# Kernel tuning notes

Measured on AMD Instinct MI355X. Metric: run time of the kernel, lower is better.

The kernel has to match this reference:

```python
import jax, jax.numpy as jnp
import numpy as np

B, NE, NR, D1, D2, L = 64, 40000, 500, 200, 200, 64
BN_EPS = 1e-5


def _batchnorm(x, gamma, beta):
    # training-mode BatchNorm1d: biased batch statistics over axis 0
    mu = jnp.mean(x, axis=0)
    var = jnp.var(x, axis=0)
    return gamma * (x - mu) * jax.lax.rsqrt(var + BN_EPS) + beta


def setup_inputs() -> dict:
    key = jax.random.key(0)
    ks = jax.random.split(key, 10)
    return {
        "e1_idx": jax.random.randint(ks[0], (B,), 0, NE),
        "r_idx": jax.random.randint(ks[1], (B,), 0, NR),
        "E": jax.random.normal(ks[2], (NE, D1), dtype=jnp.float32),
        "R": jax.random.normal(ks[3], (NR, D2), dtype=jnp.float32),
        # W ~ Uniform(-1, 1) as in the torch module
        "W": jax.random.uniform(ks[4], (D2, D1, D1), dtype=jnp.float32, minval=-1.0, maxval=1.0),
        # literals normalized into [0, 1]
        "lits": jax.random.uniform(ks[5], (NE, L), dtype=jnp.float32),
        "c": jax.random.normal(ks[6], (L,), dtype=jnp.float32) * 0.1,
        # variance buffer must be positive
        "var_l": jax.random.uniform(ks[7], (L,), dtype=jnp.float32, minval=0.5, maxval=1.5),
        "nf": jax.random.normal(ks[8], (NR, L), dtype=jnp.float32) * 0.1,
        "bn0_gamma": jnp.ones((D1,), jnp.float32),
        "bn0_beta": jnp.zeros((D1,), jnp.float32),
        "bn1_gamma": jnp.ones((D1,), jnp.float32),
        "bn1_beta": jnp.zeros((D1,), jnp.float32),
    }


def reference(e1_idx, r_idx, E, R, W, lits, c, var_l, nf,
              bn0_gamma, bn0_beta, bn1_gamma, bn1_beta):
    # --- TuckER core ---
    e1 = E[e1_idx]                                   # (B, d1)
    x = _batchnorm(e1, bn0_gamma, bn0_beta)          # (B, d1)
    r = R[r_idx]                                     # (B, d2)
    W_mat = jnp.einsum('bk,kij->bij', r, W)          # (B, d1, d1)
    x = jnp.einsum('bi,bij->bj', x, W_mat)           # (B, d1)
    x = _batchnorm(x, bn1_gamma, bn1_beta)
    score_l = x @ E.T                                # (B, N)

    # --- KBLN numeric-literal branch ---
    n_h = lits[e1_idx]                               # (B, L)
    # broadcast instead of .repeat: (B, 1, L) - (1, N, L) -> (B, N, L)
    n = n_h[:, None, :] - lits[None, :, :]
    phi = jnp.exp(-jnp.square(n - c) / var_l)        # (B, N, L)
    w_nf = nf[r_idx]                                 # (B, L)
    score_n = jnp.einsum('bnl,bl->bn', phi, w_nf)    # (B, N)

    return jax.nn.sigmoid(score_l + score_n)
```

## Files before the change

### kernel.cpp

```cpp
#include <hip/hip_runtime.h>
#include <math.h>

#define BB    64
#define NEC   40000
#define NRC   500
#define D1C   200
#define D2C   200
#define LLC   64
#define BN_EPS 1e-5f
#define LOG2E 1.4426950408889634f

#define WS_XT    0
#define WS_RT    12800
#define WS_TAP   25600
#define WS_WP    29696
#define WS_SL    33792
#define WS_X2BH  33856
#define WS_X2BL  42048
#define WS_Y     50240

typedef short s8v __attribute__((ext_vector_type(8)));
typedef float f4v __attribute__((ext_vector_type(4)));

__device__ __forceinline__ unsigned short bf16_rne(float x) {
  unsigned b = __float_as_uint(x);
  unsigned r = b + 0x7FFFu + ((b >> 16) & 1u);
  return (unsigned short)(r >> 16);
}
__device__ __forceinline__ void split2(float x, unsigned short& h,
                                       unsigned short& l) {
  h = bf16_rne(x);
  float hf = __uint_as_float(((unsigned)h) << 16);
  l = bf16_rne(x - hf);
}

__global__ __launch_bounds__(256) void prep_kernel(
    const int* __restrict__ e1_idx, const int* __restrict__ r_idx,
    const float* __restrict__ E, const float* __restrict__ R,
    const float* __restrict__ lits, const float* __restrict__ c,
    const float* __restrict__ var_l, const float* __restrict__ nf,
    const float* __restrict__ bn0g, const float* __restrict__ bn0b,
    float* __restrict__ ws) {
  float* xT  = ws + WS_XT;
  float* rT  = ws + WS_RT;
  float* taP = ws + WS_TAP;
  float* wP  = ws + WS_WP;
  float* sl  = ws + WS_SL;
  int tid = threadIdx.x;

  if (blockIdx.x == 0) {
    if (tid < D1C) {
      int j = tid;
      float ev[64];
      float sum = 0.f, sq = 0.f;
#pragma unroll
      for (int b = 0; b < BB; b++) {
        float e = E[e1_idx[b] * D1C + j];
        ev[b] = e;
        sum += e; sq += e * e;
      }
      float mean = sum * (1.f / 64.f);
      float var  = sq  * (1.f / 64.f) - mean * mean;
      float inv  = __builtin_amdgcn_rsqf(var + BN_EPS);
      float g    = bn0g[j] * inv;
      float be   = bn0b[j] - mean * g;
#pragma unroll
      for (int b = 0; b < BB; b++) {
        xT[j * 64 + b] = g * ev[b] + be;
      }
    }
  } else if (blockIdx.x == 1) {
    for (int idx = tid; idx < D2C * 64; idx += 256) {
      int k = idx >> 6, b = idx & 63;
      rT[idx] = R[r_idx[b] * D2C + k];
    }
  } else if (blockIdx.x == 2) {
    for (int idx = tid; idx < LLC * 64; idx += 256) {
      int l = idx >> 6, b = idx & 63;
      float s = sqrtf(LOG2E / var_l[l]);
      float a = (lits[e1_idx[b] * LLC + l] - c[l]) * s;
      int bp = (b & 15) * 4 + (b >> 4);
      taP[l * 64 + bp] = a + a;
      wP[l * 64 + bp]  = nf[r_idx[b] * LLC + l] * __builtin_amdgcn_exp2f(-a * a);
    }
    if (tid < LLC) sl[tid] = sqrtf(LOG2E / var_l[tid]);
  } else {
    unsigned* z = (unsigned*)(ws + WS_X2BH);
    for (int i = tid; i < 16384; i += 256) z[i] = 0u;
  }
}

__global__ __launch_bounds__(512) void stage1_kernel(
    const float* __restrict__ W, const float* __restrict__ ws_in,
    float* __restrict__ y) {
  const float* xT = ws_in + WS_XT;
  const float* rT = ws_in + WS_RT;

  int k = blockIdx.x;
  int tid = threadIdx.x;
  int lane = tid & 63;
  int w = __builtin_amdgcn_readfirstlane(tid >> 6);
  int jc = w & 3, bh = w >> 2;
  int j4 = lane & 15, bq = lane >> 4;
  int j0 = jc * 64 + j4 * 4;
  int b0 = bh * 32 + bq * 8;
  bool jok = j0 < 200;
  int joff = jok ? j0 : 0;
  const float* Wk = W + k * 40000 + joff;
  const float* xp = xT + b0;

  float acc[4][8];
#pragma unroll
  for (int jj = 0; jj < 4; jj++)
#pragma unroll
    for (int bb = 0; bb < 8; bb++) acc[jj][bb] = 0.f;

#pragma unroll 4
  for (int i = 0; i < D1C; i++) {
    float4 wv  = *(const float4*)(Wk + i * 200);
    float4 xa  = *(const float4*)(xp + i * 64);
    float4 xb2 = *(const float4*)(xp + i * 64 + 4);
    float wc[4] = {wv.x, wv.y, wv.z, wv.w};
    float xv[8] = {xa.x, xa.y, xa.z, xa.w, xb2.x, xb2.y, xb2.z, xb2.w};
#pragma unroll
    for (int jj = 0; jj < 4; jj++)
#pragma unroll
      for (int bb = 0; bb < 8; bb++)
        acc[jj][bb] += wc[jj] * xv[bb];
  }

  if (jok) {
    float4 r0 = *(const float4*)(rT + k * 64 + b0);
    float4 r1 = *(const float4*)(rT + k * 64 + b0 + 4);
    float rv[8] = {r0.x, r0.y, r0.z, r0.w, r1.x, r1.y, r1.z, r1.w};
#pragma unroll
    for (int jj = 0; jj < 4; jj++) {
      float* yo = y + (k * D1C + j0 + jj) * 64 + b0;
      float4 o0 = make_float4(acc[jj][0] * rv[0], acc[jj][1] * rv[1],
                              acc[jj][2] * rv[2], acc[jj][3] * rv[3]);
      float4 o1 = make_float4(acc[jj][4] * rv[4], acc[jj][5] * rv[5],
                              acc[jj][6] * rv[6], acc[jj][7] * rv[7]);
      *(float4*)(yo) = o0;
      *(float4*)(yo + 4) = o1;
    }
  }
}

__global__ __launch_bounds__(256) void reduce_bn1_kernel(
    const float* __restrict__ y, const float* __restrict__ bn1g,
    const float* __restrict__ bn1b, float* __restrict__ ws) {
  int j = blockIdx.x;
  int tid = threadIdx.x, b = tid & 63, kq = tid >> 6;

  float s = 0.f;
  const float* yp = y + (kq * 50 * D1C + j) * 64 + b;
#pragma unroll 10
  for (int k = 0; k < 50; k++) s += yp[k * D1C * 64];

  __shared__ float part[256];
  part[tid] = s;
  __syncthreads();
  if (tid < 64) {
    float v = part[tid] + part[64 + tid] + part[128 + tid] + part[192 + tid];
    float sum = v, sq = v * v;
#pragma unroll
    for (int o = 32; o > 0; o >>= 1) {
      sum += __shfl_xor(sum, o, 64);
      sq  += __shfl_xor(sq,  o, 64);
    }
    float mean = sum * (1.f / 64.f);
    float var  = sq  * (1.f / 64.f) - mean * mean;
    float inv  = __builtin_amdgcn_rsqf(var + BN_EPS);
    float g    = bn1g[j] * inv;
    float be   = bn1b[j] - mean * g;
    float xv   = g * v + be;
    unsigned short h, l;
    split2(xv, h, l);
    unsigned short* xh = (unsigned short*)(ws + WS_X2BH);
    unsigned short* xl = (unsigned short*)(ws + WS_X2BL);
    xh[tid * 256 + j] = h;
    xl[tid * 256 + j] = l;
  }
}

__global__ __launch_bounds__(256, 4) void final_kernel(
    const float* __restrict__ E, const float* __restrict__ lits,
    const float* __restrict__ ws, float* __restrict__ out) {
  const float* taP = ws + WS_TAP;
  const float* wP  = ws + WS_WP;
  const float* sl  = ws + WS_SL;
  const unsigned short* x2bh = (const unsigned short*)(ws + WS_X2BH);
  const unsigned short* x2bl = (const unsigned short*)(ws + WS_X2BL);

  __shared__ float SM[9216];
  unsigned short* Ah = (unsigned short*)SM;
  unsigned short* Al = Ah + 4608;
  unsigned short* Bh = Ah + 9216;
  unsigned short* Bl = Ah + 13824;

  int n0 = blockIdx.x * 64;
  int tid = threadIdx.x;
  int lane = tid & 63;
  int w = __builtin_amdgcn_readfirstlane(tid >> 6);
  int ln = lane & 15;
  int quad = lane >> 4;

  f4v acc[4];
#pragma unroll
  for (int t = 0; t < 4; t++) acc[t] = (f4v){0.f, 0.f, 0.f, 0.f};

  for (int q = 0; q < 4; q++) {
    int k0 = q * 64;
    __syncthreads();
#pragma unroll
    for (int it = 0; it < 4; it++) {
      int idx = tid + it * 256;
      int row = idx >> 4, c4 = idx & 15, cc = c4 * 4;
      float4 v = make_float4(0.f, 0.f, 0.f, 0.f);
      if (k0 + cc < 200) v = *(const float4*)(E + (n0 + row) * D1C + k0 + cc);
      unsigned short h0, l0, h1, l1, h2, l2, h3, l3;
      split2(v.x, h0, l0); split2(v.y, h1, l1);
      split2(v.z, h2, l2); split2(v.w, h3, l3);
      *(ushort4*)(Ah + row * 72 + cc) = make_ushort4(h0, h1, h2, h3);
      *(ushort4*)(Al + row * 72 + cc) = make_ushort4(l0, l1, l2, l3);
    }
#pragma unroll
    for (int it = 0; it < 4; it++) {
      int idx = tid + it * 256;
      int row = idx >> 4, c4 = idx & 15;
      *(ushort4*)(Bh + row * 72 + c4 * 4) =
          *(const ushort4*)(x2bh + row * 256 + k0 + c4 * 4);
      *(ushort4*)(Bl + row * 72 + c4 * 4) =
          *(const ushort4*)(x2bl + row * 256 + k0 + c4 * 4);
    }
    __syncthreads();

    const unsigned short* Ab  = Ah + (16 * w + ln) * 72 + quad * 8;
    const unsigned short* Alb = Al + (16 * w + ln) * 72 + quad * 8;
#pragma unroll
    for (int ks = 0; ks < 64; ks += 32) {
      s8v ah = *(const s8v*)(Ab + ks);
      s8v al = *(const s8v*)(Alb + ks);
#pragma unroll
      for (int t = 0; t < 4; t++) {
        s8v bh = *(const s8v*)(Bh + (16 * t + ln) * 72 + quad * 8 + ks);
        s8v bl = *(const s8v*)(Bl + (16 * t + ln) * 72 + quad * 8 + ks);
        acc[t] = __builtin_amdgcn_mfma_f32_16x16x32_bf16(ah, bh, acc[t], 0, 0, 0);
        acc[t] = __builtin_amdgcn_mfma_f32_16x16x32_bf16(al, bh, acc[t], 0, 0, 0);
        acc[t] = __builtin_amdgcn_mfma_f32_16x16x32_bf16(ah, bl, acc[t], 0, 0, 0);
      }
    }
  }

  float* Llds = SM;
  float* TAl  = SM + 4352;
  float* Wl   = SM + 6400;
  int nlb = 16 * w + 4 * quad;

  __syncthreads();
#pragma unroll
  for (int it = 0; it < 4; it++) {
    int idx = tid + it * 256;
    int row = idx >> 4, c4 = idx & 15;
    float4 v = *(const float4*)(lits + (n0 + row) * LLC + c4 * 4);
    int l = c4 * 4;
    Llds[(l + 0) * 68 + row] = v.x * sl[l + 0];
    Llds[(l + 1) * 68 + row] = v.y * sl[l + 1];
    Llds[(l + 2) * 68 + row] = v.z * sl[l + 2];
    Llds[(l + 3) * 68 + row] = v.w * sl[l + 3];
  }

  for (int h = 0; h < 2; h++) {
    __syncthreads();
#pragma unroll
    for (int it = 0; it < 2; it++) {
      int idx = tid + it * 256;
      ((float4*)TAl)[idx] = ((const float4*)(taP + h * 2048))[idx];
      ((float4*)Wl)[idx]  = ((const float4*)(wP  + h * 2048))[idx];
    }
    __syncthreads();
    for (int ll = 0; ll < 32; ll++) {
      float4 Lv = *(const float4*)(Llds + (h * 32 + ll) * 68 + nlb);
      float4 ta = *(const float4*)(TAl + ll * 64 + 4 * ln);
      float4 wv = *(const float4*)(Wl  + ll * 64 + 4 * ln);
      float Lc[4]  = {Lv.x, Lv.y, Lv.z, Lv.w};
      float tac[4] = {ta.x, ta.y, ta.z, ta.w};
      float wvc[4] = {wv.x, wv.y, wv.z, wv.w};
      float n2[4];
#pragma unroll
      for (int r = 0; r < 4; r++) n2[r] = -Lc[r] * Lc[r];
#pragma unroll
      for (int t = 0; t < 4; t++) {
#pragma unroll
        for (int r = 0; r < 4; r++) {
          acc[t][r] += wvc[t] *
              __builtin_amdgcn_exp2f(__builtin_fmaf(tac[t], Lc[r], n2[r]));
        }
      }
    }
  }

#pragma unroll
  for (int t = 0; t < 4; t++) {
    float4 o;
    o.x = __builtin_amdgcn_rcpf(1.f + __builtin_amdgcn_exp2f(-LOG2E * acc[t][0]));
    o.y = __builtin_amdgcn_rcpf(1.f + __builtin_amdgcn_exp2f(-LOG2E * acc[t][1]));
    o.z = __builtin_amdgcn_rcpf(1.f + __builtin_amdgcn_exp2f(-LOG2E * acc[t][2]));
    o.w = __builtin_amdgcn_rcpf(1.f + __builtin_amdgcn_exp2f(-LOG2E * acc[t][3]));
    *(float4*)(out + (size_t)(16 * t + ln) * NEC + n0 + nlb) = o;
  }
}

extern "C" void kernel_launch(void* const* d_in, const int* in_sizes, int n_in,
                              void* d_out, int out_size, void* d_ws, size_t ws_size,
                              hipStream_t stream) {
  (void)in_sizes; (void)n_in; (void)out_size; (void)ws_size;
  const int*   e1    = (const int*)d_in[0];
  const int*   ri    = (const int*)d_in[1];
  const float* E     = (const float*)d_in[2];
  const float* R     = (const float*)d_in[3];
  const float* W     = (const float*)d_in[4];
  const float* lits  = (const float*)d_in[5];
  const float* c     = (const float*)d_in[6];
  const float* var_l = (const float*)d_in[7];
  const float* nf    = (const float*)d_in[8];
  const float* bn0g  = (const float*)d_in[9];
  const float* bn0b  = (const float*)d_in[10];
  const float* bn1g  = (const float*)d_in[11];
  const float* bn1b  = (const float*)d_in[12];
  float* out = (float*)d_out;
  float* ws  = (float*)d_ws;
  float* y   = ws + WS_Y;

  prep_kernel<<<4, 256, 0, stream>>>(e1, ri, E, R, lits, c, var_l, nf,
                                     bn0g, bn0b, ws);
  stage1_kernel<<<200, 512, 0, stream>>>(W, ws, y);
  reduce_bn1_kernel<<<200, 256, 0, stream>>>(y, bn1g, bn1b, ws);
  final_kernel<<<625, 256, 0, stream>>>(E, lits, ws, out);
}
```

Measured before the change: 213.2 us.

## Split stage1 reduction over i into four chunks and prefetch loads

Stage1 now launches a 200x4 grid in which each block reduces over 50 of the 200 i values and writes partial results into a y buffer four times larger. The reduce kernel widens to 512 threads and sums the 800 partials per j. A software-pipelined register prefetch of the next W and x loads is added, and launch_bounds requests more resident waves. The aim is to fill more of the GPU's CUs, since 200 blocks underuse MI355X, at the cost of four times more intermediate y traffic and register pressure from the prefetch.

```diff
diff --git a/kernel.cpp b/kernel.cpp
--- a/kernel.cpp
+++ b/kernel.cpp
@@ -90,13 +90,14 @@
   }
 }
 
-__global__ __launch_bounds__(512) void stage1_kernel(
+__global__ __launch_bounds__(512, 6) void stage1_kernel(
     const float* __restrict__ W, const float* __restrict__ ws_in,
     float* __restrict__ y) {
   const float* xT = ws_in + WS_XT;
   const float* rT = ws_in + WS_RT;
 
   int k = blockIdx.x;
+  int ih = blockIdx.y;
   int tid = threadIdx.x;
   int lane = tid & 63;
   int w = __builtin_amdgcn_readfirstlane(tid >> 6);
@@ -106,8 +107,8 @@
   int b0 = bh * 32 + bq * 8;
   bool jok = j0 < 200;
   int joff = jok ? j0 : 0;
-  const float* Wk = W + k * 40000 + joff;
-  const float* xp = xT + b0;
+  const float* Wk = W + k * 40000 + ih * 50 * 200 + joff;
+  const float* xp = xT + ih * 50 * 64 + b0;
 
   float acc[4][8];
 #pragma unroll
@@ -115,11 +116,17 @@
 #pragma unroll
     for (int bb = 0; bb < 8; bb++) acc[jj][bb] = 0.f;
 
-#pragma unroll 4
-  for (int i = 0; i < D1C; i++) {
-    float4 wv  = *(const float4*)(Wk + i * 200);
-    float4 xa  = *(const float4*)(xp + i * 64);
-    float4 xb2 = *(const float4*)(xp + i * 64 + 4);
+  float4 wv  = *(const float4*)(Wk);
+  float4 xa  = *(const float4*)(xp);
+  float4 xb2 = *(const float4*)(xp + 4);
+#pragma unroll 5
+  for (int i = 0; i < 50; i++) {
+    float4 wv_n, xa_n, xb_n;
+    if (i < 49) {
+      wv_n = *(const float4*)(Wk + (i + 1) * 200);
+      xa_n = *(const float4*)(xp + (i + 1) * 64);
+      xb_n = *(const float4*)(xp + (i + 1) * 64 + 4);
+    }
     float wc[4] = {wv.x, wv.y, wv.z, wv.w};
     float xv[8] = {xa.x, xa.y, xa.z, xa.w, xb2.x, xb2.y, xb2.z, xb2.w};
 #pragma unroll
@@ -127,6 +134,7 @@
 #pragma unroll
       for (int bb = 0; bb < 8; bb++)
         acc[jj][bb] += wc[jj] * xv[bb];
+    wv = wv_n; xa = xa_n; xb2 = xb_n;
   }
 
   if (jok) {
@@ -135,7 +143,7 @@
     float rv[8] = {r0.x, r0.y, r0.z, r0.w, r1.x, r1.y, r1.z, r1.w};
 #pragma unroll
     for (int jj = 0; jj < 4; jj++) {
-      float* yo = y + (k * D1C + j0 + jj) * 64 + b0;
+      float* yo = y + (((ih * 200 + k) * D1C) + j0 + jj) * 64 + b0;
       float4 o0 = make_float4(acc[jj][0] * rv[0], acc[jj][1] * rv[1],
                               acc[jj][2] * rv[2], acc[jj][3] * rv[3]);
       float4 o1 = make_float4(acc[jj][4] * rv[4], acc[jj][5] * rv[5],
@@ -146,22 +154,24 @@
   }
 }
 
-__global__ __launch_bounds__(256) void reduce_bn1_kernel(
+__global__ __launch_bounds__(512) void reduce_bn1_kernel(
     const float* __restrict__ y, const float* __restrict__ bn1g,
     const float* __restrict__ bn1b, float* __restrict__ ws) {
   int j = blockIdx.x;
   int tid = threadIdx.x, b = tid & 63, kq = tid >> 6;
 
   float s = 0.f;
-  const float* yp = y + (kq * 50 * D1C + j) * 64 + b;
+  const float* yp = y + ((kq * 100) * D1C + j) * 64 + b;
 #pragma unroll 10
-  for (int k = 0; k < 50; k++) s += yp[k * D1C * 64];
-
-  __shared__ float part[256];
+  for (int k = 0; k < 100; k++) s += yp[k * D1C * 64];
+
+  __shared__ float part[512];
   part[tid] = s;
   __syncthreads();
   if (tid < 64) {
-    float v = part[tid] + part[64 + tid] + part[128 + tid] + part[192 + tid];
+    float v = part[tid]       + part[64 + tid]  + part[128 + tid] +
+              part[192 + tid] + part[256 + tid] + part[320 + tid] +
+              part[384 + tid] + part[448 + tid];
     float sum = v, sq = v * v;
 #pragma unroll
     for (int o = 32; o > 0; o >>= 1) {
@@ -178,8 +188,8 @@
     split2(xv, h, l);
     unsigned short* xh = (unsigned short*)(ws + WS_X2BH);
     unsigned short* xl = (unsigned short*)(ws + WS_X2BL);
-    xh[tid * 256 + j] = h;
-    xl[tid * 256 + j] = l;
+    xh[b * 256 + j] = h;
+    xl[b * 256 + j] = l;
   }
 }
 
@@ -334,7 +344,7 @@
 
   prep_kernel<<<4, 256, 0, stream>>>(e1, ri, E, R, lits, c, var_l, nf,
                                      bn0g, bn0b, ws);
-  stage1_kernel<<<200, 512, 0, stream>>>(W, ws, y);
-  reduce_bn1_kernel<<<200, 256, 0, stream>>>(y, bn1g, bn1b, ws);
+  stage1_kernel<<<dim3(200, 4), 512, 0, stream>>>(W, ws, y);
+  reduce_bn1_kernel<<<200, 512, 0, stream>>>(y, bn1g, bn1b, ws);
   final_kernel<<<625, 256, 0, stream>>>(E, lits, ws, out);
 }
```

Result: slower. 274.9 us (+29.0%).
